# Kernel optimization log

Measured on AMD Instinct MI355X. Metric: run time of the kernel, lower is better.

## Reference

```python
import jax, jax.numpy as jnp
import numpy as np

H = 8          # number of heads
D_MODEL = 512  # model dim
D_HEAD = D_MODEL // H


def setup_inputs() -> dict:
    key = jax.random.key(0)
    ks = jax.random.split(key, 8)
    B, C, L = 4, D_MODEL, 2048
    s = 1.0 / np.sqrt(D_MODEL)
    return {
        "x1": jax.random.normal(ks[0], (B, C, L), dtype=jnp.float32),
        "x2": jax.random.normal(ks[1], (B, C, L), dtype=jnp.float32),
        "Wq": jax.random.uniform(ks[2], (D_MODEL, D_MODEL), jnp.float32, -s, s),
        "bq": jax.random.uniform(ks[3], (D_MODEL,), jnp.float32, -s, s),
        "Wk": jax.random.uniform(ks[4], (D_MODEL, D_MODEL), jnp.float32, -s, s),
        "bk": jax.random.uniform(ks[5], (D_MODEL,), jnp.float32, -s, s),
        "Wv": jax.random.uniform(ks[6], (D_MODEL, D_MODEL), jnp.float32, -s, s),
        "bv": jax.random.uniform(ks[7], (D_MODEL,), jnp.float32, -s, s),
    }


def reference(x1, x2, Wq, bq, Wk, bk, Wv, bv):
    # x1, x2: [B, C, L] with C == d_model (3D branch of the torch module)
    B, C, L = x1.shape
    x1t = jnp.swapaxes(x1, 1, 2)  # [B, L, C]
    x2t = jnp.swapaxes(x2, 1, 2)  # [B, L, C]

    def proj(x, W, b):  # torch Linear: x @ W.T + b, then split heads
        y = jnp.einsum('blc,dc->bld', x, W) + b          # [B, L, C]
        return y.reshape(B, -1, H, D_HEAD).transpose(0, 2, 1, 3)  # [B, H, L, d]

    q = proj(x1t, Wq, bq)
    k = proj(x2t, Wk, bk)
    v = proj(x2t, Wv, bv)

    scores = jnp.einsum('bhqd,bhkd->bhqk', q, k) / jnp.sqrt(
        jnp.asarray(D_HEAD, dtype=q.dtype))
    attn = jax.nn.softmax(scores, axis=-1)
    out = jnp.einsum('bhqk,bhkd->bhqd', attn, v)          # [B, H, L, d]

    # transpose(1,2).view(B,-1,C).transpose(1,2) -> [B, C, L]
    out = out.transpose(0, 2, 1, 3).reshape(B, L, C)
    return jnp.swapaxes(out, 1, 2)
```

## Files before the change

### kernel.cpp

```cpp
#include <hip/hip_runtime.h>
#include <hip/hip_bf16.h>

#define L_SEQ 2048
#define DM 512

typedef short bf16x8 __attribute__((ext_vector_type(8)));
typedef float f32x4 __attribute__((ext_vector_type(4)));
typedef float f32x16 __attribute__((ext_vector_type(16)));
typedef unsigned short u16;
typedef u16 u16x8 __attribute__((ext_vector_type(8)));
typedef u16 u16x4 __attribute__((ext_vector_type(4)));

__device__ __forceinline__ u16 f2bf(float f) {
    unsigned int u = __float_as_uint(f);
    u += 0x7fffu + ((u >> 16) & 1u);
    return (u16)(u >> 16);
}

__device__ __forceinline__ unsigned int pk_bf16(float a, float b) {
    __hip_bfloat162 h = __float22bfloat162_rn(float2{a, b});
    unsigned int u;
    __builtin_memcpy(&u, &h, 4);
    return u;
}

__device__ __forceinline__ void lds_load16(const void* g, void* l) {
    __builtin_amdgcn_global_load_lds(
        (const __attribute__((address_space(1))) unsigned int*)g,
        (__attribute__((address_space(3))) unsigned int*)l,
        16, 0, 0);
}

__device__ __forceinline__ f32x16 zero16() {
    f32x16 z;
#pragma unroll
    for (int i = 0; i < 16; ++i) z[i] = 0.f;
    return z;
}

__global__ void cvt_w(const float* __restrict__ Wq, const float* __restrict__ Wk,
                      const float* __restrict__ Wv, u16* __restrict__ dst) {
    int i = blockIdx.x * blockDim.x + threadIdx.x;
    int which = i >> 16, j = i & 65535;
    const float* src = (which == 0) ? Wq : (which == 1 ? Wk : Wv);
    float4 v = ((const float4*)src)[j];
    ushort4 o;
    o.x = f2bf(v.x); o.y = f2bf(v.y); o.z = f2bf(v.z); o.w = f2bf(v.w);
    ((ushort4*)dst)[i] = o;
}

__global__ void tr_cvt_x(const float* __restrict__ x1, const float* __restrict__ x2,
                         u16* __restrict__ dst) {
    __shared__ u16 t[128 * 136];
    const int z = blockIdx.z, b = z & 3, c0 = blockIdx.y * 128, l0 = blockIdx.x * 128;
    const float* src = (z < 4) ? x1 : x2;
    u16* dbase = dst + (size_t)(z >> 2) * 4194304;
    const int tid = threadIdx.x;
    const float* sp = src + ((size_t)b * DM + c0) * L_SEQ + l0;
#pragma unroll
    for (int p = 0; p < 16; ++p) {
        int id = p * 256 + tid;
        int ci = id >> 5, f4 = id & 31;
        float4 v = *(const float4*)(sp + (size_t)ci * L_SEQ + f4 * 4);
        u16x4 o;
        o[0] = f2bf(v.x); o[1] = f2bf(v.y); o[2] = f2bf(v.z); o[3] = f2bf(v.w);
        *(u16x4*)(t + ci * 136 + f4 * 4) = o;
    }
    __syncthreads();
    u16* dp = dbase + ((size_t)b * L_SEQ + l0) * DM + c0;
#pragma unroll
    for (int p = 0; p < 8; ++p) {
        int id = p * 256 + tid;
        int lj = id >> 4, c8 = id & 15;
        u16x8 o;
#pragma unroll
        for (int i = 0; i < 8; ++i) o[i] = t[(c8 * 8 + i) * 136 + lj];
        *(u16x8*)(dp + (size_t)lj * DM + c8 * 8) = o;
    }
}

__launch_bounds__(256, 2)
__global__ void proj_gemm(const u16* __restrict__ x1T, const u16* __restrict__ x2T,
                          const u16* __restrict__ Wall,
                          const float* __restrict__ bq, const float* __restrict__ bk,
                          const float* __restrict__ bv,
                          u16* __restrict__ Qo, u16* __restrict__ Ko, u16* __restrict__ Vto) {
    __shared__ __align__(16) char smem[34816];
    u16* a_lds = (u16*)smem;
    u16* b_lds = (u16*)(smem + 8192);
    const int by = blockIdx.y;
    const int b = by / 3, pj = by % 3;
    const int m0 = (blockIdx.x >> 2) * 128, n0 = (blockIdx.x & 3) * 128;
    const u16* xT = (pj == 0) ? x1T : x2T;
    const u16* W = Wall + (size_t)pj * 262144;
    const float* bias = (pj == 0) ? bq : (pj == 1 ? bk : bv);
    const float scale = (pj == 0) ? 0.18033688011112042f : 1.0f;

    const int tid = threadIdx.x;
    const int w = tid >> 6, lane = tid & 63;
    const int lm = lane & 15, lq = lane >> 4;
    const int wrow = (w & 1) * 64, wcol = (w >> 1) * 64;

    const u16* gsrc[4];
    int loff[4];
#pragma unroll
    for (int j = 0; j < 4; ++j) {
        int s = (j & 1) * 256 + w * 64 + lane;
        int r = s >> 2, c = s & 3, cc = c ^ (r & 3);
        if (j < 2) gsrc[j] = xT + ((size_t)b * L_SEQ + m0 + r) * DM + cc * 8;
        else       gsrc[j] = W + (size_t)(n0 + r) * DM + cc * 8;
        loff[j] = ((j & 1) * 256 + w * 64) * 8;
    }

    f32x4 acc[4][4];
#pragma unroll
    for (int mt = 0; mt < 4; ++mt)
#pragma unroll
        for (int nt = 0; nt < 4; ++nt) acc[mt][nt] = (f32x4){0.f, 0.f, 0.f, 0.f};

    for (int kt = 0; kt < 16; ++kt) {
        __syncthreads();
#pragma unroll
        for (int j = 0; j < 4; ++j)
            lds_load16(gsrc[j] + kt * 32, (j < 2 ? a_lds : b_lds) + loff[j]);
        __syncthreads();
        bf16x8 af[4], bfr[4];
#pragma unroll
        for (int mt = 0; mt < 4; ++mt) {
            int r = wrow + mt * 16 + lm;
            af[mt] = *(const bf16x8*)(a_lds + r * 32 + (lq ^ (r & 3)) * 8);
        }
#pragma unroll
        for (int nt = 0; nt < 4; ++nt) {
            int r = wcol + nt * 16 + lm;
            bfr[nt] = *(const bf16x8*)(b_lds + r * 32 + (lq ^ (r & 3)) * 8);
        }
#pragma unroll
        for (int mt = 0; mt < 4; ++mt)
#pragma unroll
            for (int nt = 0; nt < 4; ++nt)
                acc[mt][nt] = __builtin_amdgcn_mfma_f32_16x16x32_bf16(af[mt], bfr[nt], acc[mt][nt], 0, 0, 0);
    }

    float bvv[4];
#pragma unroll
    for (int nt = 0; nt < 4; ++nt) bvv[nt] = bias[n0 + wcol + nt * 16 + lm];

    if (pj < 2) {
        u16* dst = (pj == 0) ? Qo : Ko;
#pragma unroll
        for (int mt = 0; mt < 4; ++mt)
#pragma unroll
            for (int nt = 0; nt < 4; ++nt) {
                int col = n0 + wcol + nt * 16 + lm;
#pragma unroll
                for (int r = 0; r < 4; ++r) {
                    int row = m0 + wrow + mt * 16 + lq * 4 + r;
                    dst[((size_t)b * L_SEQ + row) * DM + col] = f2bf((acc[mt][nt][r] + bvv[nt]) * scale);
                }
            }
    } else {
        __syncthreads();
        u16* epi = (u16*)smem;
#pragma unroll
        for (int mt = 0; mt < 4; ++mt)
#pragma unroll
            for (int nt = 0; nt < 4; ++nt) {
                int colL = wcol + nt * 16 + lm;
                int row0 = wrow + mt * 16 + lq * 4;
                u16x4 tv;
#pragma unroll
                for (int r = 0; r < 4; ++r) tv[r] = f2bf(acc[mt][nt][r] + bvv[nt]);
                *(u16x4*)(epi + colL * 136 + row0) = tv;
            }
        __syncthreads();
#pragma unroll
        for (int p = 0; p < 8; ++p) {
            int id = p * 256 + tid;
            int rr = id >> 4, ch = id & 15;
            u16x8 vv = *(const u16x8*)(epi + rr * 136 + ch * 8);
            *(u16x8*)(Vto + ((size_t)b * DM + n0 + rr) * L_SEQ + m0 + ch * 8) = vv;
        }
    }
}

__launch_bounds__(256, 3)
__global__ void attn(const u16* __restrict__ Q, const u16* __restrict__ K,
                     const u16* __restrict__ Vt, float* __restrict__ out) {
    __shared__ __align__(16) char smem[50688];
    u16* p_lds = (u16*)(smem + 32768);
    float* l_lds = (float*)(smem + 50176);
    float* o_lds = (float*)smem;

    const int i = blockIdx.x;
    const int g = i & 7, r_ = i >> 3;
    const int qb = r_ & 15, bh = ((r_ >> 4) << 3) + g;
    const int h_ = bh >> 2, b = bh & 3;

    const int tid = threadIdx.x, w = tid >> 6, lane = tid & 63;
    const int q0 = qb * 128, wr = w * 32;
    const int lm32 = lane & 31, hi = lane >> 5;
    const int qrow = wr + lm32;

    const u16* Qb = Q + ((size_t)b * L_SEQ + q0) * DM + h_ * 64;
    const u16* Kb = K + (size_t)b * L_SEQ * DM + h_ * 64;
    const u16* Vb = Vt + ((size_t)b * DM + h_ * 64) * L_SEQ;

    const u16 *gK[2], *gV[2];
    int soff[2];
#pragma unroll
    for (int j = 0; j < 2; ++j) {
        int s = j * 256 + tid;
        int r = s >> 3, c = s & 7, cc = c ^ (r & 7);
        gK[j] = Kb + (size_t)r * DM + cc * 8;
        gV[j] = Vb + (size_t)r * L_SEQ + cc * 8;
        soff[j] = (j * 256 + w * 64) * 8;
    }

#pragma unroll
    for (int j = 0; j < 4; ++j) {
        int s = j * 256 + tid;
        int r = s >> 3, c = s & 7, cc = c ^ (r & 7);
        lds_load16(Qb + (size_t)r * DM + cc * 8, (u16*)smem + (j * 256 + w * 64) * 8);
    }
    __syncthreads();
    bf16x8 qf[4];
#pragma unroll
    for (int c = 0; c < 4; ++c) {
        int slot = (2 * c + hi) ^ (qrow & 7);
        qf[c] = *(const bf16x8*)((const u16*)smem + qrow * 64 + slot * 8);
    }
    __syncthreads();

    float l_part = 0.f;
    f32x16 o_acc[2];
    o_acc[0] = zero16(); o_acc[1] = zero16();

#pragma unroll
    for (int j = 0; j < 2; ++j) {
        lds_load16(gK[j], (u16*)smem + soff[j]);
        lds_load16(gV[j], (u16*)(smem + 16384) + soff[j]);
    }

    u16* prow = p_lds + qrow * 68;

    for (int kt = 0; kt < 32; ++kt) {
        __syncthreads();
        if (kt < 31) {
            int nb = (kt + 1) & 1;
#pragma unroll
            for (int j = 0; j < 2; ++j) {
                lds_load16(gK[j] + (size_t)(kt + 1) * 64 * DM, (u16*)(smem + nb * 8192) + soff[j]);
                lds_load16(gV[j] + (kt + 1) * 64, (u16*)(smem + 16384 + nb * 8192) + soff[j]);
            }
        }
        const u16* kl = (const u16*)(smem + (kt & 1) * 8192);
        const u16* vl = (const u16*)(smem + 16384 + (kt & 1) * 8192);

#pragma unroll
        for (int kb2 = 0; kb2 < 2; ++kb2) {
            int rk = kb2 * 32 + lm32;
            f32x16 s = zero16();
#pragma unroll
            for (int c = 0; c < 4; ++c) {
                int slot = (2 * c + hi) ^ (rk & 7);
                bf16x8 af = *(const bf16x8*)(kl + rk * 64 + slot * 8);
                s = __builtin_amdgcn_mfma_f32_32x32x16_bf16(af, qf[c], s, 0, 0, 0);
            }
#pragma unroll
            for (int g2 = 0; g2 < 4; ++g2) {
                float p0 = __builtin_amdgcn_exp2f(s[4 * g2 + 0]);
                float p1 = __builtin_amdgcn_exp2f(s[4 * g2 + 1]);
                float p2 = __builtin_amdgcn_exp2f(s[4 * g2 + 2]);
                float p3 = __builtin_amdgcn_exp2f(s[4 * g2 + 3]);
                l_part += (p0 + p1) + (p2 + p3);
                uint2 pw;
                pw.x = pk_bf16(p0, p1);
                pw.y = pk_bf16(p2, p3);
                int k0 = kb2 * 32 + 8 * g2 + 4 * hi;
                *(uint2*)(prow + k0) = pw;
            }
        }

#pragma unroll
        for (int c = 0; c < 4; ++c) {
            u16x4 pa = *(const u16x4*)(prow + 16 * c + 8 * hi);
            u16x4 pb = *(const u16x4*)(prow + 16 * c + 8 * hi + 4);
            bf16x8 pf;
#pragma unroll
            for (int t2 = 0; t2 < 4; ++t2) { pf[t2] = (short)pa[t2]; pf[t2 + 4] = (short)pb[t2]; }
#pragma unroll
            for (int dt = 0; dt < 2; ++dt) {
                int d = dt * 32 + lm32;
                int slot = (2 * c + hi) ^ (d & 7);
                bf16x8 vf = *(const bf16x8*)(vl + d * 64 + slot * 8);
                o_acc[dt] = __builtin_amdgcn_mfma_f32_32x32x16_bf16(pf, vf, o_acc[dt], 0, 0, 0);
            }
        }
    }

    l_part += __shfl_xor(l_part, 32);

    __syncthreads();
    if (hi == 0) l_lds[qrow] = 1.0f / l_part;
#pragma unroll
    for (int dt = 0; dt < 2; ++dt) {
        int d = dt * 32 + lm32;
#pragma unroll
        for (int g2 = 0; g2 < 4; ++g2) {
            f32x4 vq;
#pragma unroll
            for (int r = 0; r < 4; ++r) vq[r] = o_acc[dt][4 * g2 + r];
            *(f32x4*)(o_lds + d * 132 + wr + 8 * g2 + 4 * hi) = vq;
        }
    }
    __syncthreads();
    float* ob = out + ((size_t)b * DM + h_ * 64) * L_SEQ + q0;
#pragma unroll
    for (int p = 0; p < 8; ++p) {
        int id = p * 256 + tid;
        int d = id >> 5, rc = id & 31;
        f32x4 vv = *(const f32x4*)(o_lds + d * 132 + rc * 4);
        f32x4 il = *(const f32x4*)(l_lds + rc * 4);
#pragma unroll
        for (int j = 0; j < 4; ++j) vv[j] *= il[j];
        *(f32x4*)(ob + (size_t)d * L_SEQ + rc * 4) = vv;
    }
}

extern "C" void kernel_launch(void* const* d_in, const int* in_sizes, int n_in,
                              void* d_out, int out_size, void* d_ws, size_t ws_size,
                              hipStream_t stream) {
    const float* x1 = (const float*)d_in[0];
    const float* x2 = (const float*)d_in[1];
    const float* Wq = (const float*)d_in[2];
    const float* bq = (const float*)d_in[3];
    const float* Wk = (const float*)d_in[4];
    const float* bk = (const float*)d_in[5];
    const float* Wv = (const float*)d_in[6];
    const float* bv = (const float*)d_in[7];
    float* out = (float*)d_out;

    char* ws = (char*)d_ws;
    u16* x1T = (u16*)(ws);
    u16* x2T = (u16*)(ws + 8388608);
    u16* Wall = (u16*)(ws + 16777216);
    u16* Qb  = (u16*)(ws + 18350080);
    u16* Kb  = (u16*)(ws + 26738688);
    u16* Vtb = (u16*)(ws + 35127296);

    cvt_w<<<768, 256, 0, stream>>>(Wq, Wk, Wv, Wall);
    tr_cvt_x<<<dim3(16, 4, 8), 256, 0, stream>>>(x1, x2, x1T);
    proj_gemm<<<dim3(64, 12), 256, 0, stream>>>(x1T, x2T, Wall, bq, bk, bv, Qb, Kb, Vtb);
    attn<<<512, 256, 0, stream>>>(Qb, Kb, Vtb, out);
}
```

Baseline: 166.6 us.

## Fuse prep kernels, double-buffer projection GEMM, split attention keys across waves

Merges the weight and input conversion kernels into one launch, saving a kernel launch. The projection GEMM now double-buffers its LDS tiles so the next k-slice loads while the current one computes, and its occupancy hint goes from 2 to 3. The attention kernel moves to 512 threads, where two wave groups each take half of every key block. The P tile is passed between lanes with shuffles instead of an LDS round trip, and the two partial outputs and row sums are reduced through LDS at the end. This adds an extra reduction pass and uses more threads per block.

```diff
diff --git a/kernel.cpp b/kernel.cpp
--- a/kernel.cpp
+++ b/kernel.cpp
@@ -38,24 +38,29 @@
     return z;
 }
 
-__global__ void cvt_w(const float* __restrict__ Wq, const float* __restrict__ Wk,
-                      const float* __restrict__ Wv, u16* __restrict__ dst) {
-    int i = blockIdx.x * blockDim.x + threadIdx.x;
-    int which = i >> 16, j = i & 65535;
-    const float* src = (which == 0) ? Wq : (which == 1 ? Wk : Wv);
-    float4 v = ((const float4*)src)[j];
-    ushort4 o;
-    o.x = f2bf(v.x); o.y = f2bf(v.y); o.z = f2bf(v.z); o.w = f2bf(v.w);
-    ((ushort4*)dst)[i] = o;
-}
-
-__global__ void tr_cvt_x(const float* __restrict__ x1, const float* __restrict__ x2,
-                         u16* __restrict__ dst) {
+__global__ void prep(const float* __restrict__ x1, const float* __restrict__ x2,
+                     const float* __restrict__ Wq, const float* __restrict__ Wk,
+                     const float* __restrict__ Wv,
+                     u16* __restrict__ xT, u16* __restrict__ Wall) {
     __shared__ u16 t[128 * 136];
+    const int tid = threadIdx.x;
+    if (blockIdx.z == 8) {
+        int gid = (blockIdx.y * 16 + blockIdx.x) * 256 + tid;
+#pragma unroll
+        for (int p = 0; p < 12; ++p) {
+            int i = p * 16384 + gid;
+            int which = i >> 16, j = i & 65535;
+            const float* src = (which == 0) ? Wq : (which == 1 ? Wk : Wv);
+            float4 v = ((const float4*)src)[j];
+            ushort4 o;
+            o.x = f2bf(v.x); o.y = f2bf(v.y); o.z = f2bf(v.z); o.w = f2bf(v.w);
+            ((ushort4*)Wall)[i] = o;
+        }
+        return;
+    }
     const int z = blockIdx.z, b = z & 3, c0 = blockIdx.y * 128, l0 = blockIdx.x * 128;
     const float* src = (z < 4) ? x1 : x2;
-    u16* dbase = dst + (size_t)(z >> 2) * 4194304;
-    const int tid = threadIdx.x;
+    u16* dbase = xT + (size_t)(z >> 2) * 4194304;
     const float* sp = src + ((size_t)b * DM + c0) * L_SEQ + l0;
 #pragma unroll
     for (int p = 0; p < 16; ++p) {
@@ -79,15 +84,13 @@
     }
 }
 
-__launch_bounds__(256, 2)
+__launch_bounds__(256, 3)
 __global__ void proj_gemm(const u16* __restrict__ x1T, const u16* __restrict__ x2T,
                           const u16* __restrict__ Wall,
                           const float* __restrict__ bq, const float* __restrict__ bk,
                           const float* __restrict__ bv,
                           u16* __restrict__ Qo, u16* __restrict__ Ko, u16* __restrict__ Vto) {
     __shared__ __align__(16) char smem[34816];
-    u16* a_lds = (u16*)smem;
-    u16* b_lds = (u16*)(smem + 8192);
     const int by = blockIdx.y;
     const int b = by / 3, pj = by % 3;
     const int m0 = (blockIdx.x >> 2) * 128, n0 = (blockIdx.x & 3) * 128;
@@ -101,15 +104,15 @@
     const int lm = lane & 15, lq = lane >> 4;
     const int wrow = (w & 1) * 64, wcol = (w >> 1) * 64;
 
-    const u16* gsrc[4];
-    int loff[4];
-#pragma unroll
-    for (int j = 0; j < 4; ++j) {
-        int s = (j & 1) * 256 + w * 64 + lane;
+    const u16* gA[2]; const u16* gB[2];
+    int adst[2];
+#pragma unroll
+    for (int j = 0; j < 2; ++j) {
+        int s = j * 256 + tid;
         int r = s >> 2, c = s & 3, cc = c ^ (r & 3);
-        if (j < 2) gsrc[j] = xT + ((size_t)b * L_SEQ + m0 + r) * DM + cc * 8;
-        else       gsrc[j] = W + (size_t)(n0 + r) * DM + cc * 8;
-        loff[j] = ((j & 1) * 256 + w * 64) * 8;
+        gA[j] = xT + ((size_t)b * L_SEQ + m0 + r) * DM + cc * 8;
+        gB[j] = W + (size_t)(n0 + r) * DM + cc * 8;
+        adst[j] = (j * 256 + w * 64) * 8;
     }
 
     f32x4 acc[4][4];
@@ -117,13 +120,25 @@
     for (int mt = 0; mt < 4; ++mt)
 #pragma unroll
         for (int nt = 0; nt < 4; ++nt) acc[mt][nt] = (f32x4){0.f, 0.f, 0.f, 0.f};
+
+#pragma unroll
+    for (int j = 0; j < 2; ++j) {
+        lds_load16(gA[j], (u16*)smem + adst[j]);
+        lds_load16(gB[j], (u16*)(smem + 8192) + adst[j]);
+    }
 
     for (int kt = 0; kt < 16; ++kt) {
         __syncthreads();
-#pragma unroll
-        for (int j = 0; j < 4; ++j)
-            lds_load16(gsrc[j] + kt * 32, (j < 2 ? a_lds : b_lds) + loff[j]);
-        __syncthreads();
+        if (kt < 15) {
+            int nb = (kt + 1) & 1;
+#pragma unroll
+            for (int j = 0; j < 2; ++j) {
+                lds_load16(gA[j] + (kt + 1) * 32, (u16*)(smem + nb * 16384) + adst[j]);
+                lds_load16(gB[j] + (kt + 1) * 32, (u16*)(smem + 8192 + nb * 16384) + adst[j]);
+            }
+        }
+        const u16* a_lds = (const u16*)(smem + (kt & 1) * 16384);
+        const u16* b_lds = (const u16*)(smem + 8192 + (kt & 1) * 16384);
         bf16x8 af[4], bfr[4];
 #pragma unroll
         for (int mt = 0; mt < 4; ++mt) {
@@ -184,12 +199,11 @@
     }
 }
 
-__launch_bounds__(256, 3)
+__launch_bounds__(512, 4)
 __global__ void attn(const u16* __restrict__ Q, const u16* __restrict__ K,
                      const u16* __restrict__ Vt, float* __restrict__ out) {
-    __shared__ __align__(16) char smem[50688];
-    u16* p_lds = (u16*)(smem + 32768);
-    float* l_lds = (float*)(smem + 50176);
+    __shared__ __align__(16) char smem[34816];
+    float* l_lds = (float*)(smem + 33792);
     float* o_lds = (float*)smem;
 
     const int i = blockIdx.x;
@@ -198,30 +212,29 @@
     const int h_ = bh >> 2, b = bh & 3;
 
     const int tid = threadIdx.x, w = tid >> 6, lane = tid & 63;
-    const int q0 = qb * 128, wr = w * 32;
+    const int q0 = qb * 128;
     const int lm32 = lane & 31, hi = lane >> 5;
-    const int qrow = wr + lm32;
+    const int qg = w & 3, hk = w >> 2;
+    const int qrow = qg * 32 + lm32;
 
     const u16* Qb = Q + ((size_t)b * L_SEQ + q0) * DM + h_ * 64;
     const u16* Kb = K + (size_t)b * L_SEQ * DM + h_ * 64;
     const u16* Vb = Vt + ((size_t)b * DM + h_ * 64) * L_SEQ;
 
-    const u16 *gK[2], *gV[2];
-    int soff[2];
+    const u16 *gK, *gV;
+    int soff;
+    {
+        int r = tid >> 3, c = tid & 7, cc = c ^ (r & 7);
+        gK = Kb + (size_t)r * DM + cc * 8;
+        gV = Vb + (size_t)r * L_SEQ + cc * 8;
+        soff = (w * 64) * 8;
+    }
+
 #pragma unroll
     for (int j = 0; j < 2; ++j) {
-        int s = j * 256 + tid;
+        int s = j * 512 + tid;
         int r = s >> 3, c = s & 7, cc = c ^ (r & 7);
-        gK[j] = Kb + (size_t)r * DM + cc * 8;
-        gV[j] = Vb + (size_t)r * L_SEQ + cc * 8;
-        soff[j] = (j * 256 + w * 64) * 8;
-    }
-
-#pragma unroll
-    for (int j = 0; j < 4; ++j) {
-        int s = j * 256 + tid;
-        int r = s >> 3, c = s & 7, cc = c ^ (r & 7);
-        lds_load16(Qb + (size_t)r * DM + cc * 8, (u16*)smem + (j * 256 + w * 64) * 8);
+        lds_load16(Qb + (size_t)r * DM + cc * 8, (u16*)smem + (j * 512 + w * 64) * 8);
     }
     __syncthreads();
     bf16x8 qf[4];
@@ -236,64 +249,58 @@
     f32x16 o_acc[2];
     o_acc[0] = zero16(); o_acc[1] = zero16();
 
-#pragma unroll
-    for (int j = 0; j < 2; ++j) {
-        lds_load16(gK[j], (u16*)smem + soff[j]);
-        lds_load16(gV[j], (u16*)(smem + 16384) + soff[j]);
-    }
-
-    u16* prow = p_lds + qrow * 68;
+    lds_load16(gK, (u16*)smem + soff);
+    lds_load16(gV, (u16*)(smem + 16384) + soff);
+
+    const int rk = hk * 32 + lm32;
 
     for (int kt = 0; kt < 32; ++kt) {
         __syncthreads();
         if (kt < 31) {
             int nb = (kt + 1) & 1;
-#pragma unroll
-            for (int j = 0; j < 2; ++j) {
-                lds_load16(gK[j] + (size_t)(kt + 1) * 64 * DM, (u16*)(smem + nb * 8192) + soff[j]);
-                lds_load16(gV[j] + (kt + 1) * 64, (u16*)(smem + 16384 + nb * 8192) + soff[j]);
-            }
+            lds_load16(gK + (size_t)(kt + 1) * 64 * DM, (u16*)(smem + nb * 8192) + soff);
+            lds_load16(gV + (kt + 1) * 64, (u16*)(smem + 16384 + nb * 8192) + soff);
         }
         const u16* kl = (const u16*)(smem + (kt & 1) * 8192);
         const u16* vl = (const u16*)(smem + 16384 + (kt & 1) * 8192);
 
-#pragma unroll
-        for (int kb2 = 0; kb2 < 2; ++kb2) {
-            int rk = kb2 * 32 + lm32;
-            f32x16 s = zero16();
-#pragma unroll
-            for (int c = 0; c < 4; ++c) {
-                int slot = (2 * c + hi) ^ (rk & 7);
-                bf16x8 af = *(const bf16x8*)(kl + rk * 64 + slot * 8);
-                s = __builtin_amdgcn_mfma_f32_32x32x16_bf16(af, qf[c], s, 0, 0, 0);
-            }
-#pragma unroll
-            for (int g2 = 0; g2 < 4; ++g2) {
-                float p0 = __builtin_amdgcn_exp2f(s[4 * g2 + 0]);
-                float p1 = __builtin_amdgcn_exp2f(s[4 * g2 + 1]);
-                float p2 = __builtin_amdgcn_exp2f(s[4 * g2 + 2]);
-                float p3 = __builtin_amdgcn_exp2f(s[4 * g2 + 3]);
-                l_part += (p0 + p1) + (p2 + p3);
-                uint2 pw;
-                pw.x = pk_bf16(p0, p1);
-                pw.y = pk_bf16(p2, p3);
-                int k0 = kb2 * 32 + 8 * g2 + 4 * hi;
-                *(uint2*)(prow + k0) = pw;
-            }
-        }
-
+        f32x16 s = zero16();
 #pragma unroll
         for (int c = 0; c < 4; ++c) {
-            u16x4 pa = *(const u16x4*)(prow + 16 * c + 8 * hi);
-            u16x4 pb = *(const u16x4*)(prow + 16 * c + 8 * hi + 4);
+            int slot = (2 * c + hi) ^ (rk & 7);
+            bf16x8 af = *(const bf16x8*)(kl + rk * 64 + slot * 8);
+            s = __builtin_amdgcn_mfma_f32_32x32x16_bf16(af, qf[c], s, 0, 0, 0);
+        }
+        uint2 pw[4];
+#pragma unroll
+        for (int g2 = 0; g2 < 4; ++g2) {
+            float p0 = __builtin_amdgcn_exp2f(s[4 * g2 + 0]);
+            float p1 = __builtin_amdgcn_exp2f(s[4 * g2 + 1]);
+            float p2 = __builtin_amdgcn_exp2f(s[4 * g2 + 2]);
+            float p3 = __builtin_amdgcn_exp2f(s[4 * g2 + 3]);
+            l_part += (p0 + p1) + (p2 + p3);
+            pw[g2].x = pk_bf16(p0, p1);
+            pw[g2].y = pk_bf16(p2, p3);
+        }
+
+#pragma unroll
+        for (int c2 = 0; c2 < 2; ++c2) {
+            uint2 pa = pw[2 * c2], pb = pw[2 * c2 + 1];
+            uint2 kep, snd;
+            if (hi) { kep = pb; snd = pa; } else { kep = pa; snd = pb; }
+            uint2 rcv;
+            rcv.x = __shfl_xor(snd.x, 32);
+            rcv.y = __shfl_xor(snd.y, 32);
+            uint4 pu;
+            if (hi) { pu.x = rcv.x; pu.y = rcv.y; pu.z = kep.x; pu.w = kep.y; }
+            else    { pu.x = kep.x; pu.y = kep.y; pu.z = rcv.x; pu.w = rcv.y; }
             bf16x8 pf;
-#pragma unroll
-            for (int t2 = 0; t2 < 4; ++t2) { pf[t2] = (short)pa[t2]; pf[t2 + 4] = (short)pb[t2]; }
+            __builtin_memcpy(&pf, &pu, 16);
 #pragma unroll
             for (int dt = 0; dt < 2; ++dt) {
                 int d = dt * 32 + lm32;
-                int slot = (2 * c + hi) ^ (d & 7);
-                bf16x8 vf = *(const bf16x8*)(vl + d * 64 + slot * 8);
+                int kc = hk * 4 + c2 * 2 + hi;
+                bf16x8 vf = *(const bf16x8*)(vl + d * 64 + (kc ^ (d & 7)) * 8);
                 o_acc[dt] = __builtin_amdgcn_mfma_f32_32x32x16_bf16(pf, vf, o_acc[dt], 0, 0, 0);
             }
         }
@@ -302,28 +309,46 @@
     l_part += __shfl_xor(l_part, 32);
 
     __syncthreads();
-    if (hi == 0) l_lds[qrow] = 1.0f / l_part;
-#pragma unroll
-    for (int dt = 0; dt < 2; ++dt) {
-        int d = dt * 32 + lm32;
-#pragma unroll
-        for (int g2 = 0; g2 < 4; ++g2) {
-            f32x4 vq;
-#pragma unroll
-            for (int r = 0; r < 4; ++r) vq[r] = o_acc[dt][4 * g2 + r];
-            *(f32x4*)(o_lds + d * 132 + wr + 8 * g2 + 4 * hi) = vq;
+    if (hi == 0) l_lds[hk * 128 + qrow] = l_part;
+    if (hk == 0) {
+#pragma unroll
+        for (int dt = 0; dt < 2; ++dt) {
+            int d = dt * 32 + lm32;
+#pragma unroll
+            for (int g2 = 0; g2 < 4; ++g2) {
+                f32x4 vq;
+#pragma unroll
+                for (int r = 0; r < 4; ++r) vq[r] = o_acc[dt][4 * g2 + r];
+                *(f32x4*)(o_lds + d * 132 + qg * 32 + 8 * g2 + 4 * hi) = vq;
+            }
+        }
+    }
+    __syncthreads();
+    if (hk == 1) {
+#pragma unroll
+        for (int dt = 0; dt < 2; ++dt) {
+            int d = dt * 32 + lm32;
+#pragma unroll
+            for (int g2 = 0; g2 < 4; ++g2) {
+                float* ad = o_lds + d * 132 + qg * 32 + 8 * g2 + 4 * hi;
+                f32x4 cur = *(f32x4*)ad;
+#pragma unroll
+                for (int r = 0; r < 4; ++r) cur[r] += o_acc[dt][4 * g2 + r];
+                *(f32x4*)ad = cur;
+            }
         }
     }
     __syncthreads();
     float* ob = out + ((size_t)b * DM + h_ * 64) * L_SEQ + q0;
 #pragma unroll
-    for (int p = 0; p < 8; ++p) {
-        int id = p * 256 + tid;
+    for (int p = 0; p < 4; ++p) {
+        int id = p * 512 + tid;
         int d = id >> 5, rc = id & 31;
         f32x4 vv = *(const f32x4*)(o_lds + d * 132 + rc * 4);
-        f32x4 il = *(const f32x4*)(l_lds + rc * 4);
-#pragma unroll
-        for (int j = 0; j < 4; ++j) vv[j] *= il[j];
+        f32x4 la = *(const f32x4*)(l_lds + rc * 4);
+        f32x4 lb = *(const f32x4*)(l_lds + 128 + rc * 4);
+#pragma unroll
+        for (int j = 0; j < 4; ++j) vv[j] *= 1.0f / (la[j] + lb[j]);
         *(f32x4*)(ob + (size_t)d * L_SEQ + rc * 4) = vv;
     }
 }
@@ -349,8 +374,7 @@
     u16* Kb  = (u16*)(ws + 26738688);
     u16* Vtb = (u16*)(ws + 35127296);
 
-    cvt_w<<<768, 256, 0, stream>>>(Wq, Wk, Wv, Wall);
-    tr_cvt_x<<<dim3(16, 4, 8), 256, 0, stream>>>(x1, x2, x1T);
+    prep<<<dim3(16, 4, 9), 256, 0, stream>>>(x1, x2, Wq, Wk, Wv, x1T, Wall);
     proj_gemm<<<dim3(64, 12), 256, 0, stream>>>(x1T, x2T, Wall, bq, bk, bv, Qb, Kb, Vtb);
-    attn<<<512, 256, 0, stream>>>(Qb, Kb, Vtb, out);
-}
+    attn<<<512, 512, 0, stream>>>(Qb, Kb, Vtb, out);
+}
```

New measurement: 167.7 us. About the same (+0.7%).
